# Kernel tuning notes

Measured on AMD Instinct MI355X. Metric: run time of the kernel, lower is better.

The kernel has to match this reference:

```python
import jax, jax.numpy as jnp
import numpy as np

HEADS = 8


def setup_inputs() -> dict:
    key = jax.random.key(0)
    ks = jax.random.split(key, 5)
    B, C, H, W = 2, 256, 48, 48
    s = 0.02
    return {
        "ct": jax.random.normal(ks[0], (B, C, H, W), jnp.float32),
        "us": jax.random.normal(ks[1], (B, C, H, W), jnp.float32),
        "w_qkv_ct": jax.random.normal(ks[2], (3 * C, C), jnp.float32) * s,
        "w_qkv_us": jax.random.normal(ks[3], (3 * C, C), jnp.float32) * s,
        "w_proj": jax.random.normal(ks[4], (C, 2 * C), jnp.float32) * s,
        "b_proj": jnp.zeros((C,), jnp.float32),
    }


def _heads_view(x, B, H, W):
    # [B, C, H, W] -> [B, heads, HW, dh]
    C = x.shape[1]
    return x.reshape(B, HEADS, C // HEADS, H * W).transpose(0, 1, 3, 2)


def _cross_attn(q, k, v, scale):
    # q,k,v: [B, heads, HW, dh]
    attn = jax.nn.softmax(jnp.einsum("bhnd,bhmd->bhnm", q, k) * scale, axis=-1)
    return jnp.einsum("bhnm,bhmd->bhnd", attn, v)


def reference(ct, us, w_qkv_ct, w_qkv_us, w_proj, b_proj):
    B, C, H, W = ct.shape
    dh = C // HEADS
    scale = dh ** (-0.5)

    # 1x1 convs as channel GEMMs
    qkv1 = jnp.einsum("oc,bchw->bohw", w_qkv_ct, ct)
    qkv2 = jnp.einsum("oc,bchw->bohw", w_qkv_us, us)
    q1, k1, v1 = jnp.split(qkv1, 3, axis=1)
    q2, k2, v2 = jnp.split(qkv2, 3, axis=1)

    # CT queries attend to US keys/values
    o1 = _cross_attn(_heads_view(q1, B, H, W), _heads_view(k2, B, H, W),
                     _heads_view(v2, B, H, W), scale)
    # US queries attend to CT keys/values
    o2 = _cross_attn(_heads_view(q2, B, H, W), _heads_view(k1, B, H, W),
                     _heads_view(v1, B, H, W), scale)

    # [B, heads, HW, dh] -> [B, C, H, W]
    out1 = o1.transpose(0, 1, 3, 2).reshape(B, C, H, W)
    out2 = o2.transpose(0, 1, 3, 2).reshape(B, C, H, W)

    fused = jnp.concatenate([ct + out1, us + out2], axis=1)
    return jnp.einsum("oc,bchw->bohw", w_proj, fused) + b_proj[None, :, None, None]
```

## Files before the change

### kernel.cpp

```cpp
#include <hip/hip_runtime.h>
#include <hip/hip_bf16.h>
#include <math.h>

#define HW   2304
#define CCH  256

#define QSCALE 0.25504368686637270f

typedef short short8 __attribute__((ext_vector_type(8)));
typedef float f32x4  __attribute__((ext_vector_type(4)));

__device__ inline unsigned short f2bf(float f) {
    union { float f; unsigned u; } v; v.f = f;
    unsigned r = v.u + 0x7FFF + ((v.u >> 16) & 1);
    return (unsigned short)(r >> 16);
}
__device__ inline unsigned pkbf2(float a, float b) {
    float2 f; f.x = a; f.y = b;
    union { __hip_bfloat162 h; unsigned u; } c;
    c.h = __float22bfloat162_rn(f);
    return c.u;
}
__device__ inline unsigned pktrunc(float a, float b) {
    return __builtin_amdgcn_perm(__builtin_bit_cast(unsigned, b),
                                 __builtin_bit_cast(unsigned, a), 0x07060302u);
}


__device__ __forceinline__ void prep_unit(
    int u, int t,
    const float* __restrict__ ct, const float* __restrict__ us,
    const float* __restrict__ w1, const float* __restrict__ w2,
    const float* __restrict__ w3,
    unsigned short* __restrict__ xT,
    unsigned short* __restrict__ wb1, unsigned short* __restrict__ wb2,
    unsigned short* __restrict__ w3b,
    unsigned short* __restrict__ Ts )
{
    if (u >= 576) {
        const int v_ = u - 576;
        int z, base;
        if (v_ < 192)      { z = 0; base = v_ * 1024; }
        else if (v_ < 384) { z = 1; base = (v_ - 192) * 1024; }
        else               { z = 2; base = (v_ - 384) * 1024; }
        const float* s = (z == 0) ? w1 : (z == 1) ? w2 : w3;
        unsigned short* d = (z == 0) ? wb1 : (z == 1) ? wb2 : w3b;
        const int i = base + t * 4;
        const float4 v4 = *(const float4*)&s[i];
        const float sc = (z < 2 && i < 65536) ? QSCALE : 1.f;
        uint2 p; p.x = pkbf2(v4.x * sc, v4.y * sc); p.y = pkbf2(v4.z * sc, v4.w * sc);
        *(uint2*)&d[i] = p;
        return;
    }
    const int pt = u % 36, rest = u / 36, ctile = rest & 3, z = rest >> 2;
    const float* __restrict__ src = ((z >> 1) ? us : ct) + (size_t)(z & 1) * CCH * HW;
    unsigned short* __restrict__ dst = xT + (size_t)z * HW * 256;
    const int p0 = pt * 64, c0 = ctile * 64;
    const int m = t & 15, ms = ((m >> 1) & 7) << 3;
    __syncthreads();
#pragma unroll
    for (int r = 0; r < 4; r++) {
        const int c = (t >> 4) + 16 * r;
        const float4 v4 = *(const float4*)&src[(size_t)(c0 + c) * HW + p0 + m * 4];
        const int cs = c ^ ms;
        Ts[(m * 4 + 0) * 72 + cs] = f2bf(v4.x);
        Ts[(m * 4 + 1) * 72 + cs] = f2bf(v4.y);
        Ts[(m * 4 + 2) * 72 + cs] = f2bf(v4.z);
        Ts[(m * 4 + 3) * 72 + cs] = f2bf(v4.w);
    }
    __syncthreads();
    const int p = t >> 2, c8 = (t & 3) * 16;
    const int es = ((p >> 3) & 7) << 3;
    const short8 a  = *(const short8*)&Ts[p * 72 + (c8 ^ es)];
    const short8 b8 = *(const short8*)&Ts[p * 72 + ((c8 + 8) ^ es)];
    *(short8*)&dst[(size_t)(p0 + p) * 256 + c0 + c8]     = a;
    *(short8*)&dst[(size_t)(p0 + p) * 256 + c0 + c8 + 8] = b8;
}

__device__ __forceinline__ void qkv_unit(
    int ptile, int otile, int z, int t,
    const unsigned short* __restrict__ xT,
    const unsigned short* __restrict__ wb1, const unsigned short* __restrict__ wb2,
    unsigned short* __restrict__ qkvT1, unsigned short* __restrict__ qkvT2,
    unsigned short* __restrict__ vdm1,  unsigned short* __restrict__ vdm2,
    unsigned short* __restrict__ Ws, unsigned short* __restrict__ Xs)
{
    const int inp = z >> 1, b = z & 1;
    const unsigned short* __restrict__ X = xT + (size_t)(inp * 2 + b) * HW * 256;
    const unsigned short* __restrict__ W = inp ? wb2 : wb1;
    unsigned short* __restrict__ qT = (inp ? qkvT2 : qkvT1) + (size_t)b * HW * 512;
    unsigned short* __restrict__ vd = (inp ? vdm2 : vdm1) + (size_t)b * CCH * HW;
    const int p0 = ptile * 64, o0 = otile * 64;
    const int w = t >> 6, lane = t & 63, quad = lane >> 4, m = lane & 15;
    const int sr = t >> 3, sc = t & 7;

    f32x4 acc[4] = {{0,0,0,0},{0,0,0,0},{0,0,0,0},{0,0,0,0}};

    short8 wv0 = *(const short8*)&W[(size_t)(o0 + sr) * 256 + sc * 8];
    short8 wv1 = *(const short8*)&W[(size_t)(o0 + 32 + sr) * 256 + sc * 8];
    short8 xv0 = *(const short8*)&X[(size_t)(p0 + sr) * 256 + sc * 8];
    short8 xv1 = *(const short8*)&X[(size_t)(p0 + 32 + sr) * 256 + sc * 8];

    for (int k0 = 0; k0 < 256; k0 += 64) {
        __syncthreads();
        *(short8*)&Ws[sr * 72 + sc * 8] = wv0;
        *(short8*)&Ws[(32 + sr) * 72 + sc * 8] = wv1;
        *(short8*)&Xs[sr * 72 + sc * 8] = xv0;
        *(short8*)&Xs[(32 + sr) * 72 + sc * 8] = xv1;
        __syncthreads();
        const int kn = k0 + 64;
        if (kn < 256) {
            wv0 = *(const short8*)&W[(size_t)(o0 + sr) * 256 + kn + sc * 8];
            wv1 = *(const short8*)&W[(size_t)(o0 + 32 + sr) * 256 + kn + sc * 8];
            xv0 = *(const short8*)&X[(size_t)(p0 + sr) * 256 + kn + sc * 8];
            xv1 = *(const short8*)&X[(size_t)(p0 + 32 + sr) * 256 + kn + sc * 8];
        }
#pragma unroll
        for (int kc2 = 0; kc2 < 2; kc2++) {
            const short8 af = *(const short8*)&Ws[(w * 16 + m) * 72 + kc2 * 32 + quad * 8];
#pragma unroll
            for (int pg = 0; pg < 4; pg++) {
                const short8 bf = *(const short8*)&Xs[(pg * 16 + m) * 72 + kc2 * 32 + quad * 8];
                acc[pg] = __builtin_amdgcn_mfma_f32_16x16x32_bf16(af, bf, acc[pg], 0, 0, 0);
            }
        }
    }
    __syncthreads();
    if (o0 < 512) {
#pragma unroll
        for (int pg = 0; pg < 4; pg++) {
            uint2 pk; pk.x = pkbf2(acc[pg][0], acc[pg][1]); pk.y = pkbf2(acc[pg][2], acc[pg][3]);
            *(uint2*)&Ws[(pg * 16 + m) * 72 + w * 16 + quad * 4] = pk;
        }
        __syncthreads();
        const int pr = t >> 2, cc = t & 3;
        const uint4 d0 = *(const uint4*)&Ws[pr * 72 + cc * 16];
        const uint4 d1 = *(const uint4*)&Ws[pr * 72 + cc * 16 + 8];
        *(uint4*)&qT[(size_t)(p0 + pr) * 512 + o0 + cc * 16]     = d0;
        *(uint4*)&qT[(size_t)(p0 + pr) * 512 + o0 + cc * 16 + 8] = d1;
    } else {
#pragma unroll
        for (int pg = 0; pg < 4; pg++)
#pragma unroll
            for (int r = 0; r < 4; r++)
                Ws[(w * 16 + quad * 4 + r) * 72 + pg * 16 + m] = f2bf(acc[pg][r]);
        __syncthreads();
        const int dr = t >> 2, cc = t & 3;
        const uint4 d0 = *(const uint4*)&Ws[dr * 72 + cc * 16];
        const uint4 d1 = *(const uint4*)&Ws[dr * 72 + cc * 16 + 8];
        *(uint4*)&vd[(size_t)(o0 - 512 + dr) * HW + p0 + cc * 16]     = d0;
        *(uint4*)&vd[(size_t)(o0 - 512 + dr) * HW + p0 + cc * 16 + 8] = d1;
    }
    __syncthreads();
}

__device__ __forceinline__ void proj_unit(
    int ptile, int otile, int t,
    const unsigned short* __restrict__ w3b, const unsigned short* __restrict__ fusedT,
    const float* __restrict__ bias, float* __restrict__ out,
    unsigned short* __restrict__ Ws, unsigned short* __restrict__ Xs)
{
    const int p0 = ptile * 64, o0 = otile * 64;
    const int w = t >> 6, lane = t & 63, quad = lane >> 4, m = lane & 15;
    const int sr = t >> 3, sc = t & 7;

    f32x4 acc[4] = {{0,0,0,0},{0,0,0,0},{0,0,0,0},{0,0,0,0}};

    short8 wv0 = *(const short8*)&w3b[(size_t)(o0 + sr) * 512 + sc * 8];
    short8 wv1 = *(const short8*)&w3b[(size_t)(o0 + 32 + sr) * 512 + sc * 8];
    short8 xv0 = *(const short8*)&fusedT[(size_t)(p0 + sr) * 512 + sc * 8];
    short8 xv1 = *(const short8*)&fusedT[(size_t)(p0 + 32 + sr) * 512 + sc * 8];

    for (int k0 = 0; k0 < 512; k0 += 64) {
        __syncthreads();
        *(short8*)&Ws[sr * 72 + sc * 8] = wv0;
        *(short8*)&Ws[(32 + sr) * 72 + sc * 8] = wv1;
        *(short8*)&Xs[sr * 72 + sc * 8] = xv0;
        *(short8*)&Xs[(32 + sr) * 72 + sc * 8] = xv1;
        __syncthreads();
        const int kn = k0 + 64;
        if (kn < 512) {
            wv0 = *(const short8*)&w3b[(size_t)(o0 + sr) * 512 + kn + sc * 8];
            wv1 = *(const short8*)&w3b[(size_t)(o0 + 32 + sr) * 512 + kn + sc * 8];
            xv0 = *(const short8*)&fusedT[(size_t)(p0 + sr) * 512 + kn + sc * 8];
            xv1 = *(const short8*)&fusedT[(size_t)(p0 + 32 + sr) * 512 + kn + sc * 8];
        }
#pragma unroll
        for (int kc2 = 0; kc2 < 2; kc2++) {
            const short8 af = *(const short8*)&Ws[(w * 16 + m) * 72 + kc2 * 32 + quad * 8];
#pragma unroll
            for (int pg = 0; pg < 4; pg++) {
                const short8 bf = *(const short8*)&Xs[(pg * 16 + m) * 72 + kc2 * 32 + quad * 8];
                acc[pg] = __builtin_amdgcn_mfma_f32_16x16x32_bf16(af, bf, acc[pg], 0, 0, 0);
            }
        }
    }
    const int b = (p0 >= HW) ? 1 : 0;
    const int pl0 = p0 - b * HW;
    float* __restrict__ ob = out + (size_t)b * CCH * HW;
    float b4[4];
#pragma unroll
    for (int r = 0; r < 4; r++) b4[r] = bias[o0 + w * 16 + quad * 4 + r];
#pragma unroll
    for (int pg = 0; pg < 4; pg++)
#pragma unroll
        for (int r = 0; r < 4; r++)
            ob[(size_t)(o0 + w * 16 + quad * 4 + r) * HW + pl0 + pg * 16 + m]
                = acc[pg][r] + b4[r];
}

__global__ __launch_bounds__(256, 4) void prep_k(
    const float* __restrict__ ct, const float* __restrict__ us,
    const float* __restrict__ w1, const float* __restrict__ w2,
    const float* __restrict__ w3,
    unsigned short* __restrict__ xT,
    unsigned short* __restrict__ b1, unsigned short* __restrict__ b2,
    unsigned short* __restrict__ b3)
{
    __shared__ __align__(16) unsigned short Ts[64 * 72];
    prep_unit(blockIdx.x, threadIdx.x, ct, us, w1, w2, w3, xT, b1, b2, b3, Ts);
}

__global__ __launch_bounds__(256, 4) void qkv_k(
    const unsigned short* __restrict__ xT,
    const unsigned short* __restrict__ wb1, const unsigned short* __restrict__ wb2,
    unsigned short* __restrict__ qkvT1, unsigned short* __restrict__ qkvT2,
    unsigned short* __restrict__ vdm1,  unsigned short* __restrict__ vdm2)
{
    __shared__ __align__(16) unsigned short Ws[64 * 72];
    __shared__ __align__(16) unsigned short Xs[64 * 72];
    const int u = (blockIdx.x & 7) * 216 + (blockIdx.x >> 3);
    const int ptile = u % 36, rest = u / 36;
    qkv_unit(ptile, rest % 12, rest / 12, threadIdx.x,
             xT, wb1, wb2, qkvT1, qkvT2, vdm1, vdm2, Ws, Xs);
}

__global__ __launch_bounds__(256, 4) void attn_k(
    const unsigned short* __restrict__ qkvT1, const unsigned short* __restrict__ qkvT2,
    const unsigned short* __restrict__ vdm1,  const unsigned short* __restrict__ vdm2,
    const float* __restrict__ ct, const float* __restrict__ us,
    unsigned short* __restrict__ fusedT)
{
    __shared__ __align__(16) unsigned short Ks[2][128 * 32];
    __shared__ __align__(16) unsigned short Vs[2][32 * 136];
    const int t = threadIdx.x;

    const int u = (blockIdx.x & 7) * 144 + (blockIdx.x >> 3);
    const int ptile = u % 36, inst = u / 36;
    const int dir = inst >> 4, b = (inst >> 3) & 1, h = inst & 7;

    const unsigned short* __restrict__ Qt = (dir ? qkvT2 : qkvT1) + (size_t)b * HW * 512;
    const unsigned short* __restrict__ Kt = (dir ? qkvT1 : qkvT2) + (size_t)b * HW * 512
                                            + 256 + h * 32;
    const unsigned short* __restrict__ Vd = (dir ? vdm1 : vdm2) + ((size_t)b * CCH + h * 32) * HW;
    const float* __restrict__ src = (dir ? us : ct) + ((size_t)b * CCH + h * 32) * HW;

    const int w = t >> 6, lane = t & 63, quad = lane >> 4, m = lane & 15;
    const int kj0 = t >> 2, kcs = t & 3;
    const int pcK = kcs ^ (((kj0 >> 1) & 1) | (((kj0 >> 3) & 1) << 1));
    const int vr0 = t >> 4, vcs = t & 15;
    const int g2m = ((m >> 1) & 1) | (((m >> 2) & 1) << 1);
    const int ksb_off = ((m >> 2) * 8 + (m & 3)) * 32 + (quad ^ g2m) * 8;
    const int vsb_off = m * 136 + quad * 8;
    const short ONE = (short)0x3F80;
    const short8 ones = {ONE,ONE,ONE,ONE,ONE,ONE,ONE,ONE};

    const int pq = ptile * 64 + w * 16 + m;
    const short8 qf = *(const short8*)&Qt[(size_t)pq * 512 + h * 32 + quad * 8];

    f32x4 acc0 = {0,0,0,0}, acc1 = {0,0,0,0}, accl = {0,0,0,0};

    short8 ka = *(const short8*)&Kt[(size_t)kj0 * 512 + kcs * 8];
    short8 kb = *(const short8*)&Kt[(size_t)(kj0 + 64) * 512 + kcs * 8];
    short8 va = *(const short8*)&Vd[(size_t)vr0 * HW + vcs * 8];
    short8 vb = *(const short8*)&Vd[(size_t)(vr0 + 16) * HW + vcs * 8];
    *(short8*)&Ks[0][kj0 * 32 + pcK * 8] = ka;
    *(short8*)&Ks[0][(kj0 + 64) * 32 + pcK * 8] = kb;
    *(short8*)&Vs[0][vr0 * 136 + vcs * 8] = va;
    *(short8*)&Vs[0][(vr0 + 16) * 136 + vcs * 8] = vb;
    ka = *(const short8*)&Kt[(size_t)(128 + kj0) * 512 + kcs * 8];
    kb = *(const short8*)&Kt[(size_t)(128 + kj0 + 64) * 512 + kcs * 8];
    va = *(const short8*)&Vd[(size_t)vr0 * HW + 128 + vcs * 8];
    vb = *(const short8*)&Vd[(size_t)(vr0 + 16) * HW + 128 + vcs * 8];
    __syncthreads();

    for (int ti = 0; ti < 18; ti++) {
        const int cur = ti & 1, nxt = cur ^ 1;
        if (ti < 17) {
            *(short8*)&Ks[nxt][kj0 * 32 + pcK * 8] = ka;
            *(short8*)&Ks[nxt][(kj0 + 64) * 32 + pcK * 8] = kb;
            *(short8*)&Vs[nxt][vr0 * 136 + vcs * 8] = va;
            *(short8*)&Vs[nxt][(vr0 + 16) * 136 + vcs * 8] = vb;
        }
        const int jn = (ti + 2) * 128;
        if (jn < HW) {
            ka = *(const short8*)&Kt[(size_t)(jn + kj0) * 512 + kcs * 8];
            kb = *(const short8*)&Kt[(size_t)(jn + kj0 + 64) * 512 + kcs * 8];
            va = *(const short8*)&Vd[(size_t)vr0 * HW + jn + vcs * 8];
            vb = *(const short8*)&Vd[(size_t)(vr0 + 16) * HW + jn + vcs * 8];
        }

        const unsigned short* __restrict__ ksb = &Ks[cur][ksb_off];
        const unsigned short* __restrict__ vsb = &Vs[cur][vsb_off];

        uint4 pw[4];
#pragma unroll
        for (int f = 0; f < 8; f++) {
            const short8 kf = *(const short8*)(ksb + ((f >> 1) * 32 + (f & 1) * 4) * 32);
            const f32x4 z = {0,0,0,0};
            const f32x4 S = __builtin_amdgcn_mfma_f32_16x16x32_bf16(kf, qf, z, 0, 0, 0);
            const float e0 = __builtin_amdgcn_exp2f(S[0]);
            const float e1 = __builtin_amdgcn_exp2f(S[1]);
            const float e2 = __builtin_amdgcn_exp2f(S[2]);
            const float e3 = __builtin_amdgcn_exp2f(S[3]);
            if ((f & 1) == 0) { pw[f >> 1].x = pktrunc(e0, e1); pw[f >> 1].y = pktrunc(e2, e3); }
            else              { pw[f >> 1].z = pktrunc(e0, e1); pw[f >> 1].w = pktrunc(e2, e3); }
        }
#pragma unroll
        for (int kt = 0; kt < 4; kt++) {
            const short8 pf = __builtin_bit_cast(short8, pw[kt]);
            const short8 vf0 = *(const short8*)(vsb + kt * 32);
            const short8 vf1 = *(const short8*)(vsb + 16 * 136 + kt * 32);
            acc0 = __builtin_amdgcn_mfma_f32_16x16x32_bf16(vf0, pf, acc0, 0, 0, 0);
            acc1 = __builtin_amdgcn_mfma_f32_16x16x32_bf16(vf1, pf, acc1, 0, 0, 0);
            accl = __builtin_amdgcn_mfma_f32_16x16x32_bf16(ones, pf, accl, 0, 0, 0);
        }
        __syncthreads();
    }

    const float inv = 1.f / accl[0];
    const int cb = dir * 256 + h * 32, d0 = quad * 4;
    unsigned short* __restrict__ fT = fusedT + ((size_t)b * HW + pq) * 512 + cb + d0;
    uint2 s0, s1;
    s0.x = pkbf2(acc0[0] * inv + src[(size_t)(d0 + 0) * HW + pq],
                 acc0[1] * inv + src[(size_t)(d0 + 1) * HW + pq]);
    s0.y = pkbf2(acc0[2] * inv + src[(size_t)(d0 + 2) * HW + pq],
                 acc0[3] * inv + src[(size_t)(d0 + 3) * HW + pq]);
    s1.x = pkbf2(acc1[0] * inv + src[(size_t)(16 + d0 + 0) * HW + pq],
                 acc1[1] * inv + src[(size_t)(16 + d0 + 1) * HW + pq]);
    s1.y = pkbf2(acc1[2] * inv + src[(size_t)(16 + d0 + 2) * HW + pq],
                 acc1[3] * inv + src[(size_t)(16 + d0 + 3) * HW + pq]);
    *(uint2*)&fT[0]  = s0;
    *(uint2*)&fT[16] = s1;
}

__global__ __launch_bounds__(256, 4) void proj_k(
    const unsigned short* __restrict__ w3b, const unsigned short* __restrict__ fusedT,
    const float* __restrict__ bias, float* __restrict__ out)
{
    __shared__ __align__(16) unsigned short Ws[64 * 72];
    __shared__ __align__(16) unsigned short Xs[64 * 72];
    const int u = (blockIdx.x & 7) * 36 + (blockIdx.x >> 3);
    proj_unit(u % 72, u / 72, threadIdx.x, w3b, fusedT, bias, out, Ws, Xs);
}

extern "C" void kernel_launch(void* const* d_in, const int* in_sizes, int n_in,
                              void* d_out, int out_size, void* d_ws, size_t ws_size,
                              hipStream_t stream)
{
    const float* ct       = (const float*)d_in[0];
    const float* us       = (const float*)d_in[1];
    const float* w_qkv_ct = (const float*)d_in[2];
    const float* w_qkv_us = (const float*)d_in[3];
    const float* w_proj   = (const float*)d_in[4];
    const float* b_proj   = (const float*)d_in[5];
    float* out = (float*)d_out;

    unsigned short* wb1   = (unsigned short*)d_ws;
    unsigned short* wb2   = wb1 + (size_t)768 * 256;
    unsigned short* w3b   = wb2 + (size_t)768 * 256;
    unsigned short* xT    = w3b + (size_t)256 * 512;
    unsigned short* qkvT1 = xT    + (size_t)4 * HW * 256;
    unsigned short* qkvT2 = qkvT1 + (size_t)2 * HW * 512;
    unsigned short* vdm1  = qkvT2 + (size_t)2 * HW * 512;
    unsigned short* vdm2  = vdm1  + (size_t)2 * CCH * HW;
    unsigned short* fusedT= vdm2  + (size_t)2 * CCH * HW;

    prep_k<<<dim3(1088), 256, 0, stream>>>(ct, us, w_qkv_ct, w_qkv_us, w_proj,
                                           xT, wb1, wb2, w3b);
    qkv_k <<<dim3(1728), 256, 0, stream>>>(xT, wb1, wb2, qkvT1, qkvT2, vdm1, vdm2);
    attn_k<<<dim3(1152), 256, 0, stream>>>(qkvT1, qkvT2, vdm1, vdm2, ct, us, fusedT);
    proj_k<<<dim3(288), 256, 0, stream>>>(w3b, fusedT, b_proj, out);
}
```

Baseline: 124.1 us.

## Split attention keys across waves with per-wave LDS tiles and final reduction

The attention kernel now has each wave own all 64 queries of the tile and process a private 32-key slice of every 128-key block. Each wave stages its own K/V slice in LDS, so the per-iteration block-wide barriers go away; partial numerators and row sums are reduced through shared memory at the end. Register pressure grows from four query groups of accumulators, so launch bounds drop to 3 blocks per SIMD. The cost is an extra cross-wave reduction and lower occupancy, and the per-wave staging is not double-buffered, so each wave waits on its own global loads.

```diff
diff --git a/kernel.cpp b/kernel.cpp
--- a/kernel.cpp
+++ b/kernel.cpp
@@ -235,14 +235,13 @@
              xT, wb1, wb2, qkvT1, qkvT2, vdm1, vdm2, Ws, Xs);
 }
 
-__global__ __launch_bounds__(256, 4) void attn_k(
+__global__ __launch_bounds__(256, 3) void attn_k(
     const unsigned short* __restrict__ qkvT1, const unsigned short* __restrict__ qkvT2,
     const unsigned short* __restrict__ vdm1,  const unsigned short* __restrict__ vdm2,
     const float* __restrict__ ct, const float* __restrict__ us,
     unsigned short* __restrict__ fusedT)
 {
-    __shared__ __align__(16) unsigned short Ks[2][128 * 32];
-    __shared__ __align__(16) unsigned short Vs[2][32 * 136];
+    __shared__ __align__(16) unsigned char smem[38912];
     const int t = threadIdx.x;
 
     const int u = (blockIdx.x & 7) * 144 + (blockIdx.x >> 3);
@@ -256,90 +255,108 @@
     const float* __restrict__ src = (dir ? us : ct) + ((size_t)b * CCH + h * 32) * HW;
 
     const int w = t >> 6, lane = t & 63, quad = lane >> 4, m = lane & 15;
-    const int kj0 = t >> 2, kcs = t & 3;
-    const int pcK = kcs ^ (((kj0 >> 1) & 1) | (((kj0 >> 3) & 1) << 1));
-    const int vr0 = t >> 4, vcs = t & 15;
+    unsigned short* __restrict__ Kq = (unsigned short*)(smem + w * 4608);
+    unsigned short* __restrict__ Vq = (unsigned short*)(smem + w * 4608 + 2048);
+
+    const int srow = lane >> 2, sslot = lane & 3;
+    const int ssk = sslot ^ (((srow >> 1) & 1) | (((srow >> 3) & 1) << 1));
     const int g2m = ((m >> 1) & 1) | (((m >> 2) & 1) << 1);
-    const int ksb_off = ((m >> 2) * 8 + (m & 3)) * 32 + (quad ^ g2m) * 8;
-    const int vsb_off = m * 136 + quad * 8;
+    const int rK  = (m >> 2) * 8 + (m & 3);
+    const unsigned short* __restrict__ ksb = &Kq[rK * 32 + (quad ^ g2m) * 8];
+    const unsigned short* __restrict__ vsb = &Vq[m * 40 + quad * 8];
     const short ONE = (short)0x3F80;
     const short8 ones = {ONE,ONE,ONE,ONE,ONE,ONE,ONE,ONE};
 
+    short8 qf[4];
+#pragma unroll
+    for (int g = 0; g < 4; g++)
+        qf[g] = *(const short8*)&Qt[(size_t)(ptile * 64 + g * 16 + m) * 512 + h * 32 + quad * 8];
+
+    f32x4 acc0[4], acc1[4], accl[4];
+#pragma unroll
+    for (int g = 0; g < 4; g++) { acc0[g] = (f32x4){0,0,0,0}; acc1[g] = (f32x4){0,0,0,0}; accl[g] = (f32x4){0,0,0,0}; }
+
+    {
+        const int j0 = w * 32;
+        const short8 ka0 = *(const short8*)&Kt[(size_t)(j0 + srow) * 512 + sslot * 8];
+        const short8 ka1 = *(const short8*)&Kt[(size_t)(j0 + srow + 16) * 512 + sslot * 8];
+        const short8 va0 = *(const short8*)&Vd[(size_t)srow * HW + j0 + sslot * 8];
+        const short8 va1 = *(const short8*)&Vd[(size_t)(srow + 16) * HW + j0 + sslot * 8];
+        *(short8*)&Kq[srow * 32 + ssk * 8]        = ka0;
+        *(short8*)&Kq[(srow + 16) * 32 + ssk * 8] = ka1;
+        *(short8*)&Vq[srow * 40 + sslot * 8]        = va0;
+        *(short8*)&Vq[(srow + 16) * 40 + sslot * 8] = va1;
+    }
+
+    for (int ti = 0; ti < 18; ti++) {
+        const short8 kf0 = *(const short8*)(ksb);
+        const short8 kf1 = *(const short8*)(ksb + 128);
+        const short8 vf0 = *(const short8*)(vsb);
+        const short8 vf1 = *(const short8*)(vsb + 16 * 40);
+        short8 ka0, ka1, va0, va1;
+        if (ti < 17) {
+            const int jn = (ti + 1) * 128 + w * 32;
+            ka0 = *(const short8*)&Kt[(size_t)(jn + srow) * 512 + sslot * 8];
+            ka1 = *(const short8*)&Kt[(size_t)(jn + srow + 16) * 512 + sslot * 8];
+            va0 = *(const short8*)&Vd[(size_t)srow * HW + jn + sslot * 8];
+            va1 = *(const short8*)&Vd[(size_t)(srow + 16) * HW + jn + sslot * 8];
+        }
+#pragma unroll
+        for (int g = 0; g < 4; g++) {
+            const f32x4 z = {0,0,0,0};
+            const f32x4 S0 = __builtin_amdgcn_mfma_f32_16x16x32_bf16(kf0, qf[g], z, 0, 0, 0);
+            const f32x4 S1 = __builtin_amdgcn_mfma_f32_16x16x32_bf16(kf1, qf[g], z, 0, 0, 0);
+            uint4 pw;
+            pw.x = pktrunc(__builtin_amdgcn_exp2f(S0[0]), __builtin_amdgcn_exp2f(S0[1]));
+            pw.y = pktrunc(__builtin_amdgcn_exp2f(S0[2]), __builtin_amdgcn_exp2f(S0[3]));
+            pw.z = pktrunc(__builtin_amdgcn_exp2f(S1[0]), __builtin_amdgcn_exp2f(S1[1]));
+            pw.w = pktrunc(__builtin_amdgcn_exp2f(S1[2]), __builtin_amdgcn_exp2f(S1[3]));
+            const short8 pf = __builtin_bit_cast(short8, pw);
+            acc0[g] = __builtin_amdgcn_mfma_f32_16x16x32_bf16(vf0, pf, acc0[g], 0, 0, 0);
+            acc1[g] = __builtin_amdgcn_mfma_f32_16x16x32_bf16(vf1, pf, acc1[g], 0, 0, 0);
+            accl[g] = __builtin_amdgcn_mfma_f32_16x16x32_bf16(ones, pf, accl[g], 0, 0, 0);
+        }
+        if (ti < 17) {
+            *(short8*)&Kq[srow * 32 + ssk * 8]        = ka0;
+            *(short8*)&Kq[(srow + 16) * 32 + ssk * 8] = ka1;
+            *(short8*)&Vq[srow * 40 + sslot * 8]        = va0;
+            *(short8*)&Vq[(srow + 16) * 40 + sslot * 8] = va1;
+        }
+    }
+
+    __syncthreads();
+    float* __restrict__ pbuf = (float*)smem;
+    float* __restrict__ plb  = (float*)(smem + 36864);
+#pragma unroll
+    for (int g = 0; g < 4; g++) {
+        float* p = &pbuf[((size_t)w * 64 + g * 16 + m) * 36 + quad * 4];
+        *(f32x4*)p        = acc0[g];
+        *(f32x4*)(p + 16) = acc1[g];
+        if (quad == 0) plb[w * 64 + g * 16 + m] = accl[g][0];
+    }
+    __syncthreads();
+    f32x4 a0 = {0,0,0,0}, a1 = {0,0,0,0};
+    float l = 0.f;
+#pragma unroll
+    for (int s = 0; s < 4; s++) {
+        const float* p = &pbuf[((size_t)s * 64 + w * 16 + m) * 36 + quad * 4];
+        a0 += *(const f32x4*)p;
+        a1 += *(const f32x4*)(p + 16);
+        l  += plb[s * 64 + w * 16 + m];
+    }
+    const float inv = 1.f / l;
     const int pq = ptile * 64 + w * 16 + m;
-    const short8 qf = *(const short8*)&Qt[(size_t)pq * 512 + h * 32 + quad * 8];
-
-    f32x4 acc0 = {0,0,0,0}, acc1 = {0,0,0,0}, accl = {0,0,0,0};
-
-    short8 ka = *(const short8*)&Kt[(size_t)kj0 * 512 + kcs * 8];
-    short8 kb = *(const short8*)&Kt[(size_t)(kj0 + 64) * 512 + kcs * 8];
-    short8 va = *(const short8*)&Vd[(size_t)vr0 * HW + vcs * 8];
-    short8 vb = *(const short8*)&Vd[(size_t)(vr0 + 16) * HW + vcs * 8];
-    *(short8*)&Ks[0][kj0 * 32 + pcK * 8] = ka;
-    *(short8*)&Ks[0][(kj0 + 64) * 32 + pcK * 8] = kb;
-    *(short8*)&Vs[0][vr0 * 136 + vcs * 8] = va;
-    *(short8*)&Vs[0][(vr0 + 16) * 136 + vcs * 8] = vb;
-    ka = *(const short8*)&Kt[(size_t)(128 + kj0) * 512 + kcs * 8];
-    kb = *(const short8*)&Kt[(size_t)(128 + kj0 + 64) * 512 + kcs * 8];
-    va = *(const short8*)&Vd[(size_t)vr0 * HW + 128 + vcs * 8];
-    vb = *(const short8*)&Vd[(size_t)(vr0 + 16) * HW + 128 + vcs * 8];
-    __syncthreads();
-
-    for (int ti = 0; ti < 18; ti++) {
-        const int cur = ti & 1, nxt = cur ^ 1;
-        if (ti < 17) {
-            *(short8*)&Ks[nxt][kj0 * 32 + pcK * 8] = ka;
-            *(short8*)&Ks[nxt][(kj0 + 64) * 32 + pcK * 8] = kb;
-            *(short8*)&Vs[nxt][vr0 * 136 + vcs * 8] = va;
-            *(short8*)&Vs[nxt][(vr0 + 16) * 136 + vcs * 8] = vb;
-        }
-        const int jn = (ti + 2) * 128;
-        if (jn < HW) {
-            ka = *(const short8*)&Kt[(size_t)(jn + kj0) * 512 + kcs * 8];
-            kb = *(const short8*)&Kt[(size_t)(jn + kj0 + 64) * 512 + kcs * 8];
-            va = *(const short8*)&Vd[(size_t)vr0 * HW + jn + vcs * 8];
-            vb = *(const short8*)&Vd[(size_t)(vr0 + 16) * HW + jn + vcs * 8];
-        }
-
-        const unsigned short* __restrict__ ksb = &Ks[cur][ksb_off];
-        const unsigned short* __restrict__ vsb = &Vs[cur][vsb_off];
-
-        uint4 pw[4];
-#pragma unroll
-        for (int f = 0; f < 8; f++) {
-            const short8 kf = *(const short8*)(ksb + ((f >> 1) * 32 + (f & 1) * 4) * 32);
-            const f32x4 z = {0,0,0,0};
-            const f32x4 S = __builtin_amdgcn_mfma_f32_16x16x32_bf16(kf, qf, z, 0, 0, 0);
-            const float e0 = __builtin_amdgcn_exp2f(S[0]);
-            const float e1 = __builtin_amdgcn_exp2f(S[1]);
-            const float e2 = __builtin_amdgcn_exp2f(S[2]);
-            const float e3 = __builtin_amdgcn_exp2f(S[3]);
-            if ((f & 1) == 0) { pw[f >> 1].x = pktrunc(e0, e1); pw[f >> 1].y = pktrunc(e2, e3); }
-            else              { pw[f >> 1].z = pktrunc(e0, e1); pw[f >> 1].w = pktrunc(e2, e3); }
-        }
-#pragma unroll
-        for (int kt = 0; kt < 4; kt++) {
-            const short8 pf = __builtin_bit_cast(short8, pw[kt]);
-            const short8 vf0 = *(const short8*)(vsb + kt * 32);
-            const short8 vf1 = *(const short8*)(vsb + 16 * 136 + kt * 32);
-            acc0 = __builtin_amdgcn_mfma_f32_16x16x32_bf16(vf0, pf, acc0, 0, 0, 0);
-            acc1 = __builtin_amdgcn_mfma_f32_16x16x32_bf16(vf1, pf, acc1, 0, 0, 0);
-            accl = __builtin_amdgcn_mfma_f32_16x16x32_bf16(ones, pf, accl, 0, 0, 0);
-        }
-        __syncthreads();
-    }
-
-    const float inv = 1.f / accl[0];
     const int cb = dir * 256 + h * 32, d0 = quad * 4;
     unsigned short* __restrict__ fT = fusedT + ((size_t)b * HW + pq) * 512 + cb + d0;
     uint2 s0, s1;
-    s0.x = pkbf2(acc0[0] * inv + src[(size_t)(d0 + 0) * HW + pq],
-                 acc0[1] * inv + src[(size_t)(d0 + 1) * HW + pq]);
-    s0.y = pkbf2(acc0[2] * inv + src[(size_t)(d0 + 2) * HW + pq],
-                 acc0[3] * inv + src[(size_t)(d0 + 3) * HW + pq]);
-    s1.x = pkbf2(acc1[0] * inv + src[(size_t)(16 + d0 + 0) * HW + pq],
-                 acc1[1] * inv + src[(size_t)(16 + d0 + 1) * HW + pq]);
-    s1.y = pkbf2(acc1[2] * inv + src[(size_t)(16 + d0 + 2) * HW + pq],
-                 acc1[3] * inv + src[(size_t)(16 + d0 + 3) * HW + pq]);
+    s0.x = pkbf2(a0[0] * inv + src[(size_t)(d0 + 0) * HW + pq],
+                 a0[1] * inv + src[(size_t)(d0 + 1) * HW + pq]);
+    s0.y = pkbf2(a0[2] * inv + src[(size_t)(d0 + 2) * HW + pq],
+                 a0[3] * inv + src[(size_t)(d0 + 3) * HW + pq]);
+    s1.x = pkbf2(a1[0] * inv + src[(size_t)(16 + d0 + 0) * HW + pq],
+                 a1[1] * inv + src[(size_t)(16 + d0 + 1) * HW + pq]);
+    s1.y = pkbf2(a1[2] * inv + src[(size_t)(16 + d0 + 2) * HW + pq],
+                 a1[3] * inv + src[(size_t)(16 + d0 + 3) * HW + pq]);
     *(uint2*)&fT[0]  = s0;
     *(uint2*)&fT[16] = s1;
 }
```

Result: no change. 123.0 us (-0.9%).
